# Kernel optimization log

Measured on AMD Instinct MI355X. Metric: run time of the kernel, lower is better.

The kernel has to match this reference:

```python
import jax, jax.numpy as jnp
import numpy as np

N_NODES = 50000
N_EDGES = 800000


def sage_conv(x, src, dst, W_l, b_l, W_r, num_nodes):
    """PyG SAGEConv with mean aggregation: out = lin_l(mean_agg(neighbors)) + lin_r(x)."""
    # gather source-node features per edge, scatter-mean into destination nodes
    msg = x[src]                                                   # [E, F]
    agg = jax.ops.segment_sum(msg, dst, num_segments=num_nodes)    # [N, F]
    cnt = jax.ops.segment_sum(jnp.ones((src.shape[0],), x.dtype), dst,
                              num_segments=num_nodes)              # [N]
    agg = agg / jnp.maximum(cnt, 1.0)[:, None]
    return agg @ W_l + b_l + x @ W_r


def setup_inputs() -> dict:
    key = jax.random.key(0)
    ks = jax.random.split(key, 8)
    d_in, d_hid, d_out = 128, 256, 128
    s = lambda k, shape, fan: jax.random.normal(k, shape, jnp.float32) / np.sqrt(fan)
    return {
        "x": jax.random.normal(ks[0], (N_NODES, d_in), jnp.float32),
        "edge_index": jax.random.randint(ks[1], (2, N_EDGES), 0, N_NODES, jnp.int64),
        "W1_l": s(ks[2], (d_in, d_hid), d_in),
        "b1": jnp.zeros((d_hid,), jnp.float32),
        "W1_r": s(ks[3], (d_in, d_hid), d_in),
        "W2_l": s(ks[4], (d_hid, d_out), d_hid),
        "b2": jnp.zeros((d_out,), jnp.float32),
        "W2_r": s(ks[5], (d_hid, d_out), d_hid),
    }


def reference(x, edge_index, W1_l, b1, W1_r, W2_l, b2, W2_r):
    src, dst = edge_index[0], edge_index[1]
    n = x.shape[0]
    h = sage_conv(x, src, dst, W1_l, b1, W1_r, n)
    h = jax.nn.relu(h)  # dropout p=0.0 -> identity
    out = sage_conv(h, src, dst, W2_l, b2, W2_r, n)
    return out
```

## Files before the change

kernel.cpp:

```cpp
#include <hip/hip_runtime.h>
#include <hip/hip_bf16.h>
#include <stdint.h>

#define NN 50000
#define NE 800000
#define NB 196
#define EPB 2048
#define NBLK ((NE + EPB - 1) / EPB)
#define BCAP 8192

typedef __attribute__((ext_vector_type(8))) __bf16 bf16x8;
typedef __attribute__((ext_vector_type(4))) float f32x4;
typedef __attribute__((ext_vector_type(4))) int i32x4;

__device__ __forceinline__ float bflo(uint32_t u) { return __uint_as_float(u << 16); }
__device__ __forceinline__ float bfhi(uint32_t u) { return __uint_as_float(u & 0xffff0000u); }
__device__ __forceinline__ uint16_t f2bf(float f) {
    uint32_t u = __float_as_uint(f);
    u += 0x7fffu + ((u >> 16) & 1u);
    return (uint16_t)(u >> 16);
}
__device__ __forceinline__ float bf2f(uint16_t h) { return __uint_as_float(((uint32_t)h) << 16); }

__device__ __forceinline__ int xcd_swz(int bid, int nwg) {
    int q = nwg >> 3, r = nwg & 7;
    int xcd = bid & 7, idx = bid >> 3;
    int base = (xcd < r) ? xcd * (q + 1) : r * (q + 1) + (xcd - r) * q;
    return base + idx;
}

__device__ __forceinline__ int detect_i64(const int* ei, int* sh_cnt) {
    int t = threadIdx.x;
    if (t == 0) *sh_cnt = 0;
    __syncthreads();
    if (t < 64) atomicAdd(sh_cnt, (ei[2 * t + 1] != 0) ? 1 : 0);
    __syncthreads();
    return (*sh_cnt < 4) ? 1 : 0;
}

__device__ __forceinline__ int detect_fp32(const uint32_t* xu, int* sh_cnt) {
    int t = threadIdx.x;
    if (t == 0) *sh_cnt = 0;
    __syncthreads();
    uint32_t u = xu[t & 255];
    uint32_t lo = u & 0xffffu;
    uint32_t e = (lo >> 7) & 0xffu;
    int ok = (lo == 0u) || (e >= 96u && e <= 150u);
    if (t < 256) atomicAdd(sh_cnt, ok);
    __syncthreads();
    return (*sh_cnt < 192) ? 1 : 0;
}

__global__ __launch_bounds__(256) void scatter1(const int* __restrict__ ei,
                                                int* __restrict__ bucket_cur,
                                                uint32_t* __restrict__ staging) {
    __shared__ int hist[NB];
    __shared__ int curs[NB];
    __shared__ int shc;
    int fl = detect_i64(ei, &shc);
    int t = threadIdx.x;
    for (int i = t; i < NB; i += 256) hist[i] = 0;
    __syncthreads();
    int base = blockIdx.x * EPB;
    for (int i = 0; i < EPB; i += 256) {
        int e = base + i + t;
        if (e < NE) {
            int d = fl ? ei[2 * NE + 2 * e] : ei[NE + e];
            atomicAdd(&hist[d >> 8], 1);
        }
    }
    __syncthreads();
    for (int i = t; i < NB; i += 256)
        curs[i] = (hist[i] > 0) ? atomicAdd(&bucket_cur[i], hist[i]) : 0;
    __syncthreads();
    for (int i = 0; i < EPB; i += 256) {
        int e = base + i + t;
        if (e < NE) {
            int s, d;
            if (fl) { s = ei[2 * e]; d = ei[2 * NE + 2 * e]; }
            else    { s = ei[e];     d = ei[NE + e]; }
            int b = d >> 8;
            int p = atomicAdd(&curs[b], 1);
            staging[b * BCAP + p] = ((uint32_t)(d & 0xff) << 16) | (uint32_t)s;
        }
    }
}

#define NORMX_BLKS 6250
__global__ __launch_bounds__(256) void csr_norm(const uint32_t* __restrict__ staging,
                                                const int* __restrict__ bucket_cur,
                                                const void* __restrict__ x,
                                                const void* __restrict__ w1l, const void* __restrict__ b1,
                                                const void* __restrict__ w1r, const void* __restrict__ w2l,
                                                const void* __restrict__ b2, const void* __restrict__ w2r,
                                                int* __restrict__ row_start, int* __restrict__ deg,
                                                float* __restrict__ inv_deg, int* __restrict__ csr,
                                                uint32_t* __restrict__ xb,
                                                uint16_t* __restrict__ w1l_sw, uint16_t* __restrict__ w1r_sw,
                                                uint16_t* __restrict__ w2l_sw, uint16_t* __restrict__ w2r_sw,
                                                uint16_t* __restrict__ bias_buf) {
    int blk = blockIdx.x;
    int t = threadIdx.x;
    if (blk < NB) {
        __shared__ int degs[256];
        __shared__ int sm[256];
        __shared__ int curs[256];
        int beg = blk * BCAP, cnt = bucket_cur[blk];
        degs[t] = 0;
        __syncthreads();
        for (int i = t; i < cnt; i += 256) atomicAdd(&degs[(staging[beg + i] >> 16) & 0xff], 1);
        __syncthreads();
        int d = degs[t];
        sm[t] = d;
        __syncthreads();
        for (int o = 1; o < 256; o <<= 1) {
            int x2 = (t >= o) ? sm[t - o] : 0;
            __syncthreads();
            sm[t] += x2;
            __syncthreads();
        }
        int excl = sm[t] - d;
        curs[t] = excl;
        int node = blk * 256 + t;
        if (node < NN) {
            row_start[node] = beg + excl;
            deg[node] = d;
            inv_deg[node] = 1.0f / (float)(d > 0 ? d : 1);
        }
        __syncthreads();
        for (int i = t; i < cnt; i += 256) {
            uint32_t u = staging[beg + i];
            int dl = (u >> 16) & 0xff;
            int p = atomicAdd(&curs[dl], 1);
            csr[beg + p] = (int)(u & 0xffffu);
        }
        return;
    }
    __shared__ int shc;
    int fp32 = detect_fp32((const uint32_t*)x, &shc);
    int nb = blk - NB;
    if (nb < NORMX_BLKS) {
        int i = nb * 256 + t;
        if (fp32) {
            f32x4 v = ((const f32x4*)x)[i];
            uint2 o;
            o.x = (uint32_t)f2bf(v[0]) | ((uint32_t)f2bf(v[1]) << 16);
            o.y = (uint32_t)f2bf(v[2]) | ((uint32_t)f2bf(v[3]) << 16);
            ((uint2*)xb)[i] = o;
        } else {
            ((uint2*)xb)[i] = ((const uint2*)x)[i];
        }
        return;
    }
    int tid = (nb - NORMX_BLKS) * 256 + t;
    if (tid < 16384) {
        int frag = tid >> 6, lane = tid & 63;
        const void* srcw; uint16_t* dst; int N; int fl;
        if (frag < 64)       { srcw = w1l; dst = w1l_sw; N = 256; fl = frag; }
        else if (frag < 128) { srcw = w1r; dst = w1r_sw; N = 256; fl = frag - 64; }
        else if (frag < 192) { srcw = w2l; dst = w2l_sw; N = 128; fl = frag - 128; }
        else                 { srcw = w2r; dst = w2r_sw; N = 128; fl = frag - 192; }
        int NTm = N >> 4;
        int kt = fl / NTm, nt = fl - kt * NTm;
        int k0 = kt * 32 + (lane >> 4) * 8, n = nt * 16 + (lane & 15);
        uint16_t* d = dst + (size_t)fl * 512 + lane * 8;
#pragma unroll
        for (int j = 0; j < 8; j++) {
            int si = (k0 + j) * N + n;
            d[j] = fp32 ? f2bf(((const float*)srcw)[si]) : ((const uint16_t*)srcw)[si];
        }
    } else if (tid < 16384 + 384) {
        int j = tid - 16384;
        const void* s = (j < 256) ? b1 : b2;
        int jj = (j < 256) ? j : j - 256;
        bias_buf[j] = fp32 ? f2bf(((const float*)s)[jj]) : ((const uint16_t*)s)[jj];
    }
}

__global__ __launch_bounds__(256) void agg_mean_v2(const uint32_t* __restrict__ xu,
                                                   const int* __restrict__ row_start,
                                                   const int* __restrict__ deg,
                                                   const int* __restrict__ csr,
                                                   const float* __restrict__ inv_deg,
                                                   uint32_t* __restrict__ outu) {
    int wave = threadIdx.x >> 6, lane = threadIdx.x & 63;
    int half = lane >> 5, l = lane & 31;
    int node = blockIdx.x * 8 + wave * 2 + half;
    int beg = row_start[node], end = beg + deg[node];
    float lx[8], hx[8], ly[8], hy[8];
#pragma unroll
    for (int k = 0; k < 8; k++) { lx[k] = 0.f; hx[k] = 0.f; ly[k] = 0.f; hy[k] = 0.f; }
    int j = beg;
    for (; j + 8 <= end; j += 8) {
        int idx[8];
#pragma unroll
        for (int k = 0; k < 8; k++) idx[k] = csr[j + k];
#pragma unroll
        for (int k = 0; k < 8; k++) {
            uint2 v = *(const uint2*)(xu + (size_t)idx[k] * 64 + l * 2);
            lx[k] += bflo(v.x); hx[k] += bfhi(v.x);
            ly[k] += bflo(v.y); hy[k] += bfhi(v.y);
        }
    }
    for (; j < end; j++) {
        uint2 v = *(const uint2*)(xu + (size_t)csr[j] * 64 + l * 2);
        lx[0] += bflo(v.x); hx[0] += bfhi(v.x);
        ly[0] += bflo(v.y); hy[0] += bfhi(v.y);
    }
    float sc = inv_deg[node];
    float r0 = (((lx[0] + lx[1]) + (lx[2] + lx[3])) + ((lx[4] + lx[5]) + (lx[6] + lx[7]))) * sc;
    float r1 = (((hx[0] + hx[1]) + (hx[2] + hx[3])) + ((hx[4] + hx[5]) + (hx[6] + hx[7]))) * sc;
    float r2 = (((ly[0] + ly[1]) + (ly[2] + ly[3])) + ((ly[4] + ly[5]) + (ly[6] + ly[7]))) * sc;
    float r3 = (((hy[0] + hy[1]) + (hy[2] + hy[3])) + ((hy[4] + hy[5]) + (hy[6] + hy[7]))) * sc;
    uint2 o;
    o.x = (uint32_t)f2bf(r0) | ((uint32_t)f2bf(r1) << 16);
    o.y = (uint32_t)f2bf(r2) | ((uint32_t)f2bf(r3) << 16);
    *(uint2*)(outu + (size_t)node * 64 + l * 2) = o;
}

__global__ __launch_bounds__(256) void agg_final_v2(const uint32_t* __restrict__ tu,
                                                    const int* __restrict__ row_start,
                                                    const int* __restrict__ deg,
                                                    const int* __restrict__ csr,
                                                    const float* __restrict__ inv_deg,
                                                    const f32x4* __restrict__ u,
                                                    f32x4* __restrict__ out) {
    int wave = threadIdx.x >> 6, lane = threadIdx.x & 63;
    int half = lane >> 5, l = lane & 31;
    int node = blockIdx.x * 8 + wave * 2 + half;
    int beg = row_start[node], end = beg + deg[node];
    float lx[8], hx[8], ly[8], hy[8];
#pragma unroll
    for (int k = 0; k < 8; k++) { lx[k] = 0.f; hx[k] = 0.f; ly[k] = 0.f; hy[k] = 0.f; }
    int j = beg;
    for (; j + 8 <= end; j += 8) {
        int idx[8];
#pragma unroll
        for (int k = 0; k < 8; k++) idx[k] = csr[j + k];
#pragma unroll
        for (int k = 0; k < 8; k++) {
            uint2 v = *(const uint2*)(tu + (size_t)idx[k] * 64 + l * 2);
            lx[k] += bflo(v.x); hx[k] += bfhi(v.x);
            ly[k] += bflo(v.y); hy[k] += bfhi(v.y);
        }
    }
    for (; j < end; j++) {
        uint2 v = *(const uint2*)(tu + (size_t)csr[j] * 64 + l * 2);
        lx[0] += bflo(v.x); hx[0] += bfhi(v.x);
        ly[0] += bflo(v.y); hy[0] += bfhi(v.y);
    }
    float sc = inv_deg[node];
    f32x4 uv = u[(size_t)node * 32 + l];
    f32x4 r;
    r[0] = (((lx[0] + lx[1]) + (lx[2] + lx[3])) + ((lx[4] + lx[5]) + (lx[6] + lx[7]))) * sc + uv[0];
    r[1] = (((hx[0] + hx[1]) + (hx[2] + hx[3])) + ((hx[4] + hx[5]) + (hx[6] + hx[7]))) * sc + uv[1];
    r[2] = (((ly[0] + ly[1]) + (ly[2] + ly[3])) + ((ly[4] + ly[5]) + (ly[6] + ly[7]))) * sc + uv[2];
    r[3] = (((hy[0] + hy[1]) + (hy[2] + hy[3])) + ((hy[4] + hy[5]) + (hy[6] + hy[7]))) * sc + uv[3];
    out[(size_t)node * 32 + l] = r;
}

__global__ __launch_bounds__(256) void gemm1_v3(const uint16_t* __restrict__ A1,
                                                const uint16_t* __restrict__ A2,
                                                const uint16_t* __restrict__ W1sw,
                                                const uint16_t* __restrict__ W2sw,
                                                const uint16_t* __restrict__ bias,
                                                uint16_t* __restrict__ C) {
    __shared__ __align__(16) uint16_t cs[64][72];
    int wg = xcd_swz(blockIdx.x, 3128);
    int rg = wg >> 2, cg = wg & 3;
    int wave = threadIdx.x >> 6, lane = threadIdx.x & 63;
    int wr = wave >> 1, wc = wave & 1;
    int m = lane & 15, q = lane >> 4;
    int rowbase = rg * 64 + wr * 32;
    int gnt0 = cg * 4 + wc * 2;

    int ar[2];
#pragma unroll
    for (int rf = 0; rf < 2; rf++) {
        int r = rowbase + rf * 16 + m;
        ar[rf] = (r < NN) ? r : (NN - 1);
    }

    bf16x8 B1[4][2], B2[4][2];
#pragma unroll
    for (int kt = 0; kt < 4; kt++)
#pragma unroll
        for (int nt = 0; nt < 2; nt++) {
            B1[kt][nt] = *(const bf16x8*)(W1sw + ((size_t)(kt * 16 + gnt0 + nt)) * 512 + lane * 8);
            B2[kt][nt] = *(const bf16x8*)(W2sw + ((size_t)(kt * 16 + gnt0 + nt)) * 512 + lane * 8);
        }

    f32x4 acc[2][2];
#pragma unroll
    for (int rf = 0; rf < 2; rf++)
#pragma unroll
        for (int nt = 0; nt < 2; nt++)
#pragma unroll
            for (int i = 0; i < 4; i++) acc[rf][nt][i] = 0.f;

#pragma unroll
    for (int kt = 0; kt < 4; kt++) {
        bf16x8 a10 = *(const bf16x8*)(A1 + (size_t)ar[0] * 128 + kt * 32 + q * 8);
        bf16x8 a11 = *(const bf16x8*)(A1 + (size_t)ar[1] * 128 + kt * 32 + q * 8);
        bf16x8 a20 = *(const bf16x8*)(A2 + (size_t)ar[0] * 128 + kt * 32 + q * 8);
        bf16x8 a21 = *(const bf16x8*)(A2 + (size_t)ar[1] * 128 + kt * 32 + q * 8);
#pragma unroll
        for (int nt = 0; nt < 2; nt++) {
            acc[0][nt] = __builtin_amdgcn_mfma_f32_16x16x32_bf16(a10, B1[kt][nt], acc[0][nt], 0, 0, 0);
            acc[1][nt] = __builtin_amdgcn_mfma_f32_16x16x32_bf16(a11, B1[kt][nt], acc[1][nt], 0, 0, 0);
            acc[0][nt] = __builtin_amdgcn_mfma_f32_16x16x32_bf16(a20, B2[kt][nt], acc[0][nt], 0, 0, 0);
            acc[1][nt] = __builtin_amdgcn_mfma_f32_16x16x32_bf16(a21, B2[kt][nt], acc[1][nt], 0, 0, 0);
        }
    }

#pragma unroll
    for (int rf = 0; rf < 2; rf++)
#pragma unroll
        for (int nt = 0; nt < 2; nt++) {
            int coll = wc * 32 + nt * 16 + m;
            float bv = bf2f(bias[cg * 64 + coll]);
#pragma unroll
            for (int i = 0; i < 4; i++) {
                float v = fmaxf(acc[rf][nt][i] + bv, 0.f);
                cs[wr * 32 + rf * 16 + q * 4 + i][coll] = f2bf(v);
            }
        }
    __syncthreads();
    int tt = threadIdx.x;
#pragma unroll
    for (int rr = 0; rr < 2; rr++) {
        int row = rr * 32 + (tt >> 3);
        int grow = rg * 64 + row;
        if (grow < NN)
            *(i32x4*)(C + (size_t)grow * 256 + cg * 64 + (tt & 7) * 8) =
                *(const i32x4*)&cs[row][(tt & 7) * 8];
    }
}

__global__ __launch_bounds__(256) void gemm2_v3(const uint16_t* __restrict__ A,
                                                const uint16_t* __restrict__ W1sw,
                                                const uint16_t* __restrict__ W2sw,
                                                const uint16_t* __restrict__ bias,
                                                uint16_t* __restrict__ T,
                                                float* __restrict__ U) {
    __shared__ __align__(16) uint16_t ts[64][72];
    __shared__ __align__(16) float us[64][68];
    int wg = xcd_swz(blockIdx.x, 1564);
    int rg = wg >> 1, cg = wg & 1;
    int wave = threadIdx.x >> 6, lane = threadIdx.x & 63;
    int wr = wave >> 1, wc = wave & 1;
    int m = lane & 15, q = lane >> 4;
    int rowbase = rg * 64 + wr * 32;
    int gnt0 = cg * 4 + wc * 2;

    int ar[2];
#pragma unroll
    for (int rf = 0; rf < 2; rf++) {
        int r = rowbase + rf * 16 + m;
        ar[rf] = (r < NN) ? r : (NN - 1);
    }

    f32x4 acc1[2][2], acc2[2][2];
#pragma unroll
    for (int rf = 0; rf < 2; rf++)
#pragma unroll
        for (int nt = 0; nt < 2; nt++)
#pragma unroll
            for (int i = 0; i < 4; i++) { acc1[rf][nt][i] = 0.f; acc2[rf][nt][i] = 0.f; }

#pragma unroll
    for (int kt = 0; kt < 8; kt++) {
        bf16x8 b10 = *(const bf16x8*)(W1sw + ((size_t)(kt * 8 + gnt0 + 0)) * 512 + lane * 8);
        bf16x8 b11 = *(const bf16x8*)(W1sw + ((size_t)(kt * 8 + gnt0 + 1)) * 512 + lane * 8);
        bf16x8 b20 = *(const bf16x8*)(W2sw + ((size_t)(kt * 8 + gnt0 + 0)) * 512 + lane * 8);
        bf16x8 b21 = *(const bf16x8*)(W2sw + ((size_t)(kt * 8 + gnt0 + 1)) * 512 + lane * 8);
        bf16x8 a0 = *(const bf16x8*)(A + (size_t)ar[0] * 256 + kt * 32 + q * 8);
        bf16x8 a1 = *(const bf16x8*)(A + (size_t)ar[1] * 256 + kt * 32 + q * 8);
        acc1[0][0] = __builtin_amdgcn_mfma_f32_16x16x32_bf16(a0, b10, acc1[0][0], 0, 0, 0);
        acc1[0][1] = __builtin_amdgcn_mfma_f32_16x16x32_bf16(a0, b11, acc1[0][1], 0, 0, 0);
        acc1[1][0] = __builtin_amdgcn_mfma_f32_16x16x32_bf16(a1, b10, acc1[1][0], 0, 0, 0);
        acc1[1][1] = __builtin_amdgcn_mfma_f32_16x16x32_bf16(a1, b11, acc1[1][1], 0, 0, 0);
        acc2[0][0] = __builtin_amdgcn_mfma_f32_16x16x32_bf16(a0, b20, acc2[0][0], 0, 0, 0);
        acc2[0][1] = __builtin_amdgcn_mfma_f32_16x16x32_bf16(a0, b21, acc2[0][1], 0, 0, 0);
        acc2[1][0] = __builtin_amdgcn_mfma_f32_16x16x32_bf16(a1, b20, acc2[1][0], 0, 0, 0);
        acc2[1][1] = __builtin_amdgcn_mfma_f32_16x16x32_bf16(a1, b21, acc2[1][1], 0, 0, 0);
    }

#pragma unroll
    for (int rf = 0; rf < 2; rf++)
#pragma unroll
        for (int nt = 0; nt < 2; nt++) {
            int coll = wc * 32 + nt * 16 + m;
            float bv = bf2f(bias[cg * 64 + coll]);
#pragma unroll
            for (int i = 0; i < 4; i++) {
                int rl = wr * 32 + rf * 16 + q * 4 + i;
                ts[rl][coll] = f2bf(acc1[rf][nt][i]);
                us[rl][coll] = acc2[rf][nt][i] + bv;
            }
        }
    __syncthreads();
    int tt = threadIdx.x;
#pragma unroll
    for (int rr = 0; rr < 2; rr++) {
        int row = rr * 32 + (tt >> 3);
        int grow = rg * 64 + row;
        if (grow < NN)
            *(i32x4*)(T + (size_t)grow * 128 + cg * 64 + (tt & 7) * 8) =
                *(const i32x4*)&ts[row][(tt & 7) * 8];
    }
#pragma unroll
    for (int rr = 0; rr < 4; rr++) {
        int row = rr * 16 + (tt >> 4);
        int grow = rg * 64 + row;
        if (grow < NN)
            *(f32x4*)(U + (size_t)grow * 128 + cg * 64 + (tt & 15) * 4) =
                *(const f32x4*)&us[row][(tt & 15) * 4];
    }
}

extern "C" void kernel_launch(void* const* d_in, const int* in_sizes, int n_in,
                              void* d_out, int out_size, void* d_ws, size_t ws_size,
                              hipStream_t stream) {
    const void* x_raw  = d_in[0];
    const int*  ei     = (const int*)d_in[1];
    const void* W1l    = d_in[2];
    const void* b1     = d_in[3];
    const void* W1r    = d_in[4];
    const void* W2l    = d_in[5];
    const void* b2     = d_in[6];
    const void* W2r    = d_in[7];

    uint8_t* ws = (uint8_t*)d_ws;
    size_t off = 0;
    auto alloc = [&](size_t b) -> void* {
        void* p = ws + off;
        off += (b + 255) & ~(size_t)255;
        return p;
    };
    int*      bucket_cur  = (int*)alloc((NB + 4) * 4);
    int*      deg         = (int*)alloc((size_t)NN * 4);
    float*    inv_deg     = (float*)alloc((size_t)NN * 4);
    int*      row_start   = (int*)alloc((size_t)NN * 4);
    int*      csr         = (int*)alloc((size_t)NB * BCAP * 4);
    uint32_t* xb          = (uint32_t*)alloc((size_t)NN * 64 * 4);
    uint16_t* bias_buf    = (uint16_t*)alloc(384 * 2);
    uint16_t* agg         = (uint16_t*)alloc((size_t)NN * 128 * 2);
    uint16_t* h           = (uint16_t*)alloc((size_t)NN * 256 * 2);
    uint16_t* t           = (uint16_t*)alloc((size_t)NN * 128 * 2);
    float*    u           = (float*)alloc((size_t)NN * 128 * 4);
    uint16_t* w1l_sw      = (uint16_t*)alloc(128 * 256 * 2);
    uint16_t* w1r_sw      = (uint16_t*)alloc(128 * 256 * 2);
    uint16_t* w2l_sw      = (uint16_t*)alloc(256 * 128 * 2);
    uint16_t* w2r_sw      = (uint16_t*)alloc(256 * 128 * 2);

    uint32_t* staging = (uint32_t*)h;

    hipMemsetAsync(bucket_cur, 0, NB * 4, stream);
    scatter1<<<NBLK, 256, 0, stream>>>(ei, bucket_cur, staging);
    csr_norm<<<NB + NORMX_BLKS + 66, 256, 0, stream>>>(staging, bucket_cur, x_raw,
                                                       W1l, b1, W1r, W2l, b2, W2r,
                                                       row_start, deg, inv_deg, csr,
                                                       xb, w1l_sw, w1r_sw, w2l_sw, w2r_sw, bias_buf);

    agg_mean_v2<<<NN / 8, 256, 0, stream>>>(xb, row_start, deg, csr, inv_deg, (uint32_t*)agg);
    gemm1_v3<<<3128, 256, 0, stream>>>(agg, (const uint16_t*)xb, w1l_sw, w1r_sw, bias_buf, h);
    gemm2_v3<<<1564, 256, 0, stream>>>(h, w2l_sw, w2r_sw, bias_buf + 256, t, u);
    agg_final_v2<<<NN / 8, 256, 0, stream>>>((const uint32_t*)t, row_start, deg, csr, inv_deg,
                                             (const f32x4*)u, (f32x4*)d_out);
}
```

Baseline: 255.6 us.

## Slice aggregation kernels by feature column, splitting edges across lanes

Both gather-mean kernels now split the 128 features into 8 column slices, one slice per block, and spread each node's edges across 8 lane groups. The partial sums are then combined with xor shuffles, and results are written with nontemporal stores. The aim is to keep each block's gather working set smaller and more cache-local, and to give more independent loads per wave. In exchange, csr indices are read 8 times and the shuffle reductions add overhead.

Result: slower. 378.4 us (+48.0%).

```diff
diff --git a/kernel.cpp b/kernel.cpp
--- a/kernel.cpp
+++ b/kernel.cpp
@@ -12,6 +12,7 @@
 typedef __attribute__((ext_vector_type(8))) __bf16 bf16x8;
 typedef __attribute__((ext_vector_type(4))) float f32x4;
 typedef __attribute__((ext_vector_type(4))) int i32x4;
+typedef __attribute__((ext_vector_type(2))) uint32_t u32x2;
 
 __device__ __forceinline__ float bflo(uint32_t u) { return __uint_as_float(u << 16); }
 __device__ __forceinline__ float bfhi(uint32_t u) { return __uint_as_float(u & 0xffff0000u); }
@@ -177,86 +178,112 @@
     }
 }
 
-__global__ __launch_bounds__(256) void agg_mean_v2(const uint32_t* __restrict__ xu,
+__global__ __launch_bounds__(256) void agg_mean_s(const uint32_t* __restrict__ xu,
+                                                  const int* __restrict__ row_start,
+                                                  const int* __restrict__ deg,
+                                                  const int* __restrict__ csr,
+                                                  const float* __restrict__ inv_deg,
+                                                  uint32_t* __restrict__ outu) {
+    int s = blockIdx.x & 7, ng = blockIdx.x >> 3;
+    int t = threadIdx.x;
+    int hw = t >> 5, l = t & 31;
+    int esub = l >> 2, dpair = l & 3;
+    int colu = s * 8 + dpair * 2;
+    for (int it = 0; it < 8; it++) {
+        int node = ng * 64 + hw * 8 + it;
+        if (node >= NN) break;
+        int beg = row_start[node], d = deg[node];
+        float f0 = 0.f, f1 = 0.f, f2 = 0.f, f3 = 0.f;
+        int j = 0;
+        for (; j + 16 <= d; j += 16) {
+            int i0 = csr[beg + j + esub];
+            int i1 = csr[beg + j + 8 + esub];
+            uint2 v0 = *(const uint2*)(xu + (size_t)i0 * 64 + colu);
+            uint2 v1 = *(const uint2*)(xu + (size_t)i1 * 64 + colu);
+            f0 += bflo(v0.x) + bflo(v1.x);
+            f1 += bfhi(v0.x) + bfhi(v1.x);
+            f2 += bflo(v0.y) + bflo(v1.y);
+            f3 += bfhi(v0.y) + bfhi(v1.y);
+        }
+        for (; j < d; j += 8) {
+            if (j + esub < d) {
+                int i0 = csr[beg + j + esub];
+                uint2 v0 = *(const uint2*)(xu + (size_t)i0 * 64 + colu);
+                f0 += bflo(v0.x); f1 += bfhi(v0.x);
+                f2 += bflo(v0.y); f3 += bfhi(v0.y);
+            }
+        }
+#pragma unroll
+        for (int mask = 4; mask <= 16; mask <<= 1) {
+            f0 += __shfl_xor(f0, mask);
+            f1 += __shfl_xor(f1, mask);
+            f2 += __shfl_xor(f2, mask);
+            f3 += __shfl_xor(f3, mask);
+        }
+        if (esub == 0) {
+            float sc = inv_deg[node];
+            u32x2 o;
+            o[0] = (uint32_t)f2bf(f0 * sc) | ((uint32_t)f2bf(f1 * sc) << 16);
+            o[1] = (uint32_t)f2bf(f2 * sc) | ((uint32_t)f2bf(f3 * sc) << 16);
+            __builtin_nontemporal_store(o, (u32x2*)(outu + (size_t)node * 64 + colu));
+        }
+    }
+}
+
+__global__ __launch_bounds__(256) void agg_final_s(const uint32_t* __restrict__ tu,
                                                    const int* __restrict__ row_start,
                                                    const int* __restrict__ deg,
                                                    const int* __restrict__ csr,
                                                    const float* __restrict__ inv_deg,
-                                                   uint32_t* __restrict__ outu) {
-    int wave = threadIdx.x >> 6, lane = threadIdx.x & 63;
-    int half = lane >> 5, l = lane & 31;
-    int node = blockIdx.x * 8 + wave * 2 + half;
-    int beg = row_start[node], end = beg + deg[node];
-    float lx[8], hx[8], ly[8], hy[8];
-#pragma unroll
-    for (int k = 0; k < 8; k++) { lx[k] = 0.f; hx[k] = 0.f; ly[k] = 0.f; hy[k] = 0.f; }
-    int j = beg;
-    for (; j + 8 <= end; j += 8) {
-        int idx[8];
-#pragma unroll
-        for (int k = 0; k < 8; k++) idx[k] = csr[j + k];
-#pragma unroll
-        for (int k = 0; k < 8; k++) {
-            uint2 v = *(const uint2*)(xu + (size_t)idx[k] * 64 + l * 2);
-            lx[k] += bflo(v.x); hx[k] += bfhi(v.x);
-            ly[k] += bflo(v.y); hy[k] += bfhi(v.y);
-        }
-    }
-    for (; j < end; j++) {
-        uint2 v = *(const uint2*)(xu + (size_t)csr[j] * 64 + l * 2);
-        lx[0] += bflo(v.x); hx[0] += bfhi(v.x);
-        ly[0] += bflo(v.y); hy[0] += bfhi(v.y);
-    }
-    float sc = inv_deg[node];
-    float r0 = (((lx[0] + lx[1]) + (lx[2] + lx[3])) + ((lx[4] + lx[5]) + (lx[6] + lx[7]))) * sc;
-    float r1 = (((hx[0] + hx[1]) + (hx[2] + hx[3])) + ((hx[4] + hx[5]) + (hx[6] + hx[7]))) * sc;
-    float r2 = (((ly[0] + ly[1]) + (ly[2] + ly[3])) + ((ly[4] + ly[5]) + (ly[6] + ly[7]))) * sc;
-    float r3 = (((hy[0] + hy[1]) + (hy[2] + hy[3])) + ((hy[4] + hy[5]) + (hy[6] + hy[7]))) * sc;
-    uint2 o;
-    o.x = (uint32_t)f2bf(r0) | ((uint32_t)f2bf(r1) << 16);
-    o.y = (uint32_t)f2bf(r2) | ((uint32_t)f2bf(r3) << 16);
-    *(uint2*)(outu + (size_t)node * 64 + l * 2) = o;
-}
-
-__global__ __launch_bounds__(256) void agg_final_v2(const uint32_t* __restrict__ tu,
-                                                    const int* __restrict__ row_start,
-                                                    const int* __restrict__ deg,
-                                                    const int* __restrict__ csr,
-                                                    const float* __restrict__ inv_deg,
-                                                    const f32x4* __restrict__ u,
-                                                    f32x4* __restrict__ out) {
-    int wave = threadIdx.x >> 6, lane = threadIdx.x & 63;
-    int half = lane >> 5, l = lane & 31;
-    int node = blockIdx.x * 8 + wave * 2 + half;
-    int beg = row_start[node], end = beg + deg[node];
-    float lx[8], hx[8], ly[8], hy[8];
-#pragma unroll
-    for (int k = 0; k < 8; k++) { lx[k] = 0.f; hx[k] = 0.f; ly[k] = 0.f; hy[k] = 0.f; }
-    int j = beg;
-    for (; j + 8 <= end; j += 8) {
-        int idx[8];
-#pragma unroll
-        for (int k = 0; k < 8; k++) idx[k] = csr[j + k];
-#pragma unroll
-        for (int k = 0; k < 8; k++) {
-            uint2 v = *(const uint2*)(tu + (size_t)idx[k] * 64 + l * 2);
-            lx[k] += bflo(v.x); hx[k] += bfhi(v.x);
-            ly[k] += bflo(v.y); hy[k] += bfhi(v.y);
-        }
-    }
-    for (; j < end; j++) {
-        uint2 v = *(const uint2*)(tu + (size_t)csr[j] * 64 + l * 2);
-        lx[0] += bflo(v.x); hx[0] += bfhi(v.x);
-        ly[0] += bflo(v.y); hy[0] += bfhi(v.y);
-    }
-    float sc = inv_deg[node];
-    f32x4 uv = u[(size_t)node * 32 + l];
-    f32x4 r;
-    r[0] = (((lx[0] + lx[1]) + (lx[2] + lx[3])) + ((lx[4] + lx[5]) + (lx[6] + lx[7]))) * sc + uv[0];
-    r[1] = (((hx[0] + hx[1]) + (hx[2] + hx[3])) + ((hx[4] + hx[5]) + (hx[6] + hx[7]))) * sc + uv[1];
-    r[2] = (((ly[0] + ly[1]) + (ly[2] + ly[3])) + ((ly[4] + ly[5]) + (ly[6] + ly[7]))) * sc + uv[2];
-    r[3] = (((hy[0] + hy[1]) + (hy[2] + hy[3])) + ((hy[4] + hy[5]) + (hy[6] + hy[7]))) * sc + uv[3];
-    out[(size_t)node * 32 + l] = r;
+                                                   const float* __restrict__ u,
+                                                   float* __restrict__ out) {
+    int s = blockIdx.x & 7, ng = blockIdx.x >> 3;
+    int t = threadIdx.x;
+    int hw = t >> 5, l = t & 31;
+    int esub = l >> 2, dpair = l & 3;
+    int colu = s * 8 + dpair * 2;
+    for (int it = 0; it < 8; it++) {
+        int node = ng * 64 + hw * 8 + it;
+        if (node >= NN) break;
+        int beg = row_start[node], d = deg[node];
+        float f0 = 0.f, f1 = 0.f, f2 = 0.f, f3 = 0.f;
+        int j = 0;
+        for (; j + 16 <= d; j += 16) {
+            int i0 = csr[beg + j + esub];
+            int i1 = csr[beg + j + 8 + esub];
+            uint2 v0 = *(const uint2*)(tu + (size_t)i0 * 64 + colu);
+            uint2 v1 = *(const uint2*)(tu + (size_t)i1 * 64 + colu);
+            f0 += bflo(v0.x) + bflo(v1.x);
+            f1 += bfhi(v0.x) + bfhi(v1.x);
+            f2 += bflo(v0.y) + bflo(v1.y);
+            f3 += bfhi(v0.y) + bfhi(v1.y);
+        }
+        for (; j < d; j += 8) {
+            if (j + esub < d) {
+                int i0 = csr[beg + j + esub];
+                uint2 v0 = *(const uint2*)(tu + (size_t)i0 * 64 + colu);
+                f0 += bflo(v0.x); f1 += bfhi(v0.x);
+                f2 += bflo(v0.y); f3 += bfhi(v0.y);
+            }
+        }
+#pragma unroll
+        for (int mask = 4; mask <= 16; mask <<= 1) {
+            f0 += __shfl_xor(f0, mask);
+            f1 += __shfl_xor(f1, mask);
+            f2 += __shfl_xor(f2, mask);
+            f3 += __shfl_xor(f3, mask);
+        }
+        if (esub == 0) {
+            float sc = inv_deg[node];
+            f32x4 uv = *(const f32x4*)(u + (size_t)node * 128 + s * 16 + dpair * 4);
+            f32x4 r;
+            r[0] = f0 * sc + uv[0];
+            r[1] = f1 * sc + uv[1];
+            r[2] = f2 * sc + uv[2];
+            r[3] = f3 * sc + uv[3];
+            __builtin_nontemporal_store(r, (f32x4*)(out + (size_t)node * 128 + s * 16 + dpair * 4));
+        }
+    }
 }
 
 __global__ __launch_bounds__(256) void gemm1_v3(const uint16_t* __restrict__ A1,
@@ -463,9 +490,10 @@
                                                        row_start, deg, inv_deg, csr,
                                                        xb, w1l_sw, w1r_sw, w2l_sw, w2r_sw, bias_buf);
 
-    agg_mean_v2<<<NN / 8, 256, 0, stream>>>(xb, row_start, deg, csr, inv_deg, (uint32_t*)agg);
+    agg_mean_s<<<8 * ((NN + 63) / 64), 256, 0, stream>>>(xb, row_start, deg, csr, inv_deg,
+                                                         (uint32_t*)agg);
     gemm1_v3<<<3128, 256, 0, stream>>>(agg, (const uint16_t*)xb, w1l_sw, w1r_sw, bias_buf, h);
     gemm2_v3<<<1564, 256, 0, stream>>>(h, w2l_sw, w2r_sw, bias_buf + 256, t, u);
-    agg_final_v2<<<NN / 8, 256, 0, stream>>>((const uint32_t*)t, row_start, deg, csr, inv_deg,
-                                             (const f32x4*)u, (f32x4*)d_out);
-}
+    agg_final_s<<<8 * ((NN + 63) / 64), 256, 0, stream>>>((const uint32_t*)t, row_start, deg, csr,
+                                                          inv_deg, u, (float*)d_out);
+}
```

## Fuse the two dense GEMM stages, keeping hidden activations in shared memory

Applied to the files above, without the earlier changes.

Replaces the two separate GEMM kernels with one fused kernel. Each block computes a 64-row tile of the layer-1 hidden activations (bias plus ReLU) into LDS, then immediately runs the layer-2 projections from LDS and writes T and U. This removes the global write and re-read of the 50000x256 hidden tensor and one kernel launch. In exchange there are fewer, heavier blocks, more accumulator registers and more LDS per block, which may lower occupancy. The edge staging buffer now aliases the T buffer.

Result: no change. 255.2 us (-0.2%).

```diff
diff --git a/kernel.cpp b/kernel.cpp
--- a/kernel.cpp
+++ b/kernel.cpp
@@ -259,163 +259,141 @@
     out[(size_t)node * 32 + l] = r;
 }
 
-__global__ __launch_bounds__(256) void gemm1_v3(const uint16_t* __restrict__ A1,
-                                                const uint16_t* __restrict__ A2,
-                                                const uint16_t* __restrict__ W1sw,
-                                                const uint16_t* __restrict__ W2sw,
-                                                const uint16_t* __restrict__ bias,
-                                                uint16_t* __restrict__ C) {
-    __shared__ __align__(16) uint16_t cs[64][72];
-    int wg = xcd_swz(blockIdx.x, 3128);
-    int rg = wg >> 2, cg = wg & 3;
-    int wave = threadIdx.x >> 6, lane = threadIdx.x & 63;
+#define HW 264
+__global__ __launch_bounds__(256) void fused_mlp(const uint16_t* __restrict__ AGG,
+                                                 const uint16_t* __restrict__ XB,
+                                                 const uint16_t* __restrict__ W1Lsw,
+                                                 const uint16_t* __restrict__ W1Rsw,
+                                                 const uint16_t* __restrict__ W2Lsw,
+                                                 const uint16_t* __restrict__ W2Rsw,
+                                                 const uint16_t* __restrict__ bias,
+                                                 uint16_t* __restrict__ T,
+                                                 float* __restrict__ U) {
+    __shared__ __align__(16) uint16_t hbuf[64 * HW];
+    int wg = xcd_swz(blockIdx.x, 782);
+    int node0 = wg * 64;
+    int tid = threadIdx.x;
+    int wave = tid >> 6, lane = tid & 63;
     int wr = wave >> 1, wc = wave & 1;
     int m = lane & 15, q = lane >> 4;
-    int rowbase = rg * 64 + wr * 32;
-    int gnt0 = cg * 4 + wc * 2;
 
     int ar[2];
 #pragma unroll
     for (int rf = 0; rf < 2; rf++) {
-        int r = rowbase + rf * 16 + m;
+        int r = node0 + wr * 32 + rf * 16 + m;
         ar[rf] = (r < NN) ? r : (NN - 1);
     }
 
-    bf16x8 B1[4][2], B2[4][2];
-#pragma unroll
-    for (int kt = 0; kt < 4; kt++)
-#pragma unroll
-        for (int nt = 0; nt < 2; nt++) {
-            B1[kt][nt] = *(const bf16x8*)(W1sw + ((size_t)(kt * 16 + gnt0 + nt)) * 512 + lane * 8);
-            B2[kt][nt] = *(const bf16x8*)(W2sw + ((size_t)(kt * 16 + gnt0 + nt)) * 512 + lane * 8);
-        }
-
-    f32x4 acc[2][2];
+    {
+        f32x4 acc[2][8];
+#pragma unroll
+        for (int rf = 0; rf < 2; rf++)
+#pragma unroll
+            for (int nt = 0; nt < 8; nt++)
+#pragma unroll
+                for (int i = 0; i < 4; i++) acc[rf][nt][i] = 0.f;
+
+#pragma unroll
+        for (int kt = 0; kt < 4; kt++) {
+            bf16x8 a10 = *(const bf16x8*)(AGG + (size_t)ar[0] * 128 + kt * 32 + q * 8);
+            bf16x8 a11 = *(const bf16x8*)(AGG + (size_t)ar[1] * 128 + kt * 32 + q * 8);
+            bf16x8 a20 = *(const bf16x8*)(XB + (size_t)ar[0] * 128 + kt * 32 + q * 8);
+            bf16x8 a21 = *(const bf16x8*)(XB + (size_t)ar[1] * 128 + kt * 32 + q * 8);
+#pragma unroll
+            for (int nt = 0; nt < 8; nt++) {
+                int gnt = wc * 8 + nt;
+                bf16x8 B1 = *(const bf16x8*)(W1Lsw + ((size_t)(kt * 16 + gnt)) * 512 + lane * 8);
+                bf16x8 B2 = *(const bf16x8*)(W1Rsw + ((size_t)(kt * 16 + gnt)) * 512 + lane * 8);
+                acc[0][nt] = __builtin_amdgcn_mfma_f32_16x16x32_bf16(a10, B1, acc[0][nt], 0, 0, 0);
+                acc[1][nt] = __builtin_amdgcn_mfma_f32_16x16x32_bf16(a11, B1, acc[1][nt], 0, 0, 0);
+                acc[0][nt] = __builtin_amdgcn_mfma_f32_16x16x32_bf16(a20, B2, acc[0][nt], 0, 0, 0);
+                acc[1][nt] = __builtin_amdgcn_mfma_f32_16x16x32_bf16(a21, B2, acc[1][nt], 0, 0, 0);
+            }
+        }
+#pragma unroll
+        for (int rf = 0; rf < 2; rf++)
+#pragma unroll
+            for (int nt = 0; nt < 8; nt++) {
+                int cl = wc * 128 + nt * 16 + m;
+                float bv = bf2f(bias[cl]);
+#pragma unroll
+                for (int i = 0; i < 4; i++) {
+                    float v = fmaxf(acc[rf][nt][i] + bv, 0.f);
+                    hbuf[(wr * 32 + rf * 16 + q * 4 + i) * HW + cl] = f2bf(v);
+                }
+            }
+    }
+    __syncthreads();
+
+    f32x4 acc1[2][4], acc2[2][4];
 #pragma unroll
     for (int rf = 0; rf < 2; rf++)
 #pragma unroll
-        for (int nt = 0; nt < 2; nt++)
-#pragma unroll
-            for (int i = 0; i < 4; i++) acc[rf][nt][i] = 0.f;
-
-#pragma unroll
-    for (int kt = 0; kt < 4; kt++) {
-        bf16x8 a10 = *(const bf16x8*)(A1 + (size_t)ar[0] * 128 + kt * 32 + q * 8);
-        bf16x8 a11 = *(const bf16x8*)(A1 + (size_t)ar[1] * 128 + kt * 32 + q * 8);
-        bf16x8 a20 = *(const bf16x8*)(A2 + (size_t)ar[0] * 128 + kt * 32 + q * 8);
-        bf16x8 a21 = *(const bf16x8*)(A2 + (size_t)ar[1] * 128 + kt * 32 + q * 8);
-#pragma unroll
-        for (int nt = 0; nt < 2; nt++) {
-            acc[0][nt] = __builtin_amdgcn_mfma_f32_16x16x32_bf16(a10, B1[kt][nt], acc[0][nt], 0, 0, 0);
-            acc[1][nt] = __builtin_amdgcn_mfma_f32_16x16x32_bf16(a11, B1[kt][nt], acc[1][nt], 0, 0, 0);
-            acc[0][nt] = __builtin_amdgcn_mfma_f32_16x16x32_bf16(a20, B2[kt][nt], acc[0][nt], 0, 0, 0);
-            acc[1][nt] = __builtin_amdgcn_mfma_f32_16x16x32_bf16(a21, B2[kt][nt], acc[1][nt], 0, 0, 0);
-        }
-    }
-
-#pragma unroll
-    for (int rf = 0; rf < 2; rf++)
-#pragma unroll
-        for (int nt = 0; nt < 2; nt++) {
-            int coll = wc * 32 + nt * 16 + m;
-            float bv = bf2f(bias[cg * 64 + coll]);
-#pragma unroll
-            for (int i = 0; i < 4; i++) {
-                float v = fmaxf(acc[rf][nt][i] + bv, 0.f);
-                cs[wr * 32 + rf * 16 + q * 4 + i][coll] = f2bf(v);
+        for (int nt = 0; nt < 4; nt++)
+#pragma unroll
+            for (int i = 0; i < 4; i++) { acc1[rf][nt][i] = 0.f; acc2[rf][nt][i] = 0.f; }
+
+#pragma unroll
+    for (int kt = 0; kt < 8; kt++) {
+        bf16x8 a0 = *(const bf16x8*)&hbuf[(wr * 32 + m) * HW + kt * 32 + q * 8];
+        bf16x8 a1 = *(const bf16x8*)&hbuf[(wr * 32 + 16 + m) * HW + kt * 32 + q * 8];
+#pragma unroll
+        for (int nt = 0; nt < 4; nt++) {
+            int gnt = wc * 4 + nt;
+            bf16x8 BL = *(const bf16x8*)(W2Lsw + ((size_t)(kt * 8 + gnt)) * 512 + lane * 8);
+            bf16x8 BR = *(const bf16x8*)(W2Rsw + ((size_t)(kt * 8 + gnt)) * 512 + lane * 8);
+            acc1[0][nt] = __builtin_amdgcn_mfma_f32_16x16x32_bf16(a0, BL, acc1[0][nt], 0, 0, 0);
+            acc1[1][nt] = __builtin_amdgcn_mfma_f32_16x16x32_bf16(a1, BL, acc1[1][nt], 0, 0, 0);
+            acc2[0][nt] = __builtin_amdgcn_mfma_f32_16x16x32_bf16(a0, BR, acc2[0][nt], 0, 0, 0);
+            acc2[1][nt] = __builtin_amdgcn_mfma_f32_16x16x32_bf16(a1, BR, acc2[1][nt], 0, 0, 0);
+        }
+    }
+    __syncthreads();
+
+    {
+        uint16_t* st = hbuf;
+#pragma unroll
+        for (int rf = 0; rf < 2; rf++)
+#pragma unroll
+            for (int nt = 0; nt < 4; nt++) {
+                int cl = wc * 64 + nt * 16 + m;
+#pragma unroll
+                for (int i = 0; i < 4; i++)
+                    st[(wr * 32 + rf * 16 + q * 4 + i) * 136 + cl] = f2bf(acc1[rf][nt][i]);
             }
-        }
-    __syncthreads();
-    int tt = threadIdx.x;
-#pragma unroll
-    for (int rr = 0; rr < 2; rr++) {
-        int row = rr * 32 + (tt >> 3);
-        int grow = rg * 64 + row;
-        if (grow < NN)
-            *(i32x4*)(C + (size_t)grow * 256 + cg * 64 + (tt & 7) * 8) =
-                *(const i32x4*)&cs[row][(tt & 7) * 8];
-    }
-}
-
-__global__ __launch_bounds__(256) void gemm2_v3(const uint16_t* __restrict__ A,
-                                                const uint16_t* __restrict__ W1sw,
-                                                const uint16_t* __restrict__ W2sw,
-                                                const uint16_t* __restrict__ bias,
-                                                uint16_t* __restrict__ T,
-                                                float* __restrict__ U) {
-    __shared__ __align__(16) uint16_t ts[64][72];
-    __shared__ __align__(16) float us[64][68];
-    int wg = xcd_swz(blockIdx.x, 1564);
-    int rg = wg >> 1, cg = wg & 1;
-    int wave = threadIdx.x >> 6, lane = threadIdx.x & 63;
-    int wr = wave >> 1, wc = wave & 1;
-    int m = lane & 15, q = lane >> 4;
-    int rowbase = rg * 64 + wr * 32;
-    int gnt0 = cg * 4 + wc * 2;
-
-    int ar[2];
-#pragma unroll
-    for (int rf = 0; rf < 2; rf++) {
-        int r = rowbase + rf * 16 + m;
-        ar[rf] = (r < NN) ? r : (NN - 1);
-    }
-
-    f32x4 acc1[2][2], acc2[2][2];
-#pragma unroll
-    for (int rf = 0; rf < 2; rf++)
-#pragma unroll
-        for (int nt = 0; nt < 2; nt++)
-#pragma unroll
-            for (int i = 0; i < 4; i++) { acc1[rf][nt][i] = 0.f; acc2[rf][nt][i] = 0.f; }
-
-#pragma unroll
-    for (int kt = 0; kt < 8; kt++) {
-        bf16x8 b10 = *(const bf16x8*)(W1sw + ((size_t)(kt * 8 + gnt0 + 0)) * 512 + lane * 8);
-        bf16x8 b11 = *(const bf16x8*)(W1sw + ((size_t)(kt * 8 + gnt0 + 1)) * 512 + lane * 8);
-        bf16x8 b20 = *(const bf16x8*)(W2sw + ((size_t)(kt * 8 + gnt0 + 0)) * 512 + lane * 8);
-        bf16x8 b21 = *(const bf16x8*)(W2sw + ((size_t)(kt * 8 + gnt0 + 1)) * 512 + lane * 8);
-        bf16x8 a0 = *(const bf16x8*)(A + (size_t)ar[0] * 256 + kt * 32 + q * 8);
-        bf16x8 a1 = *(const bf16x8*)(A + (size_t)ar[1] * 256 + kt * 32 + q * 8);
-        acc1[0][0] = __builtin_amdgcn_mfma_f32_16x16x32_bf16(a0, b10, acc1[0][0], 0, 0, 0);
-        acc1[0][1] = __builtin_amdgcn_mfma_f32_16x16x32_bf16(a0, b11, acc1[0][1], 0, 0, 0);
-        acc1[1][0] = __builtin_amdgcn_mfma_f32_16x16x32_bf16(a1, b10, acc1[1][0], 0, 0, 0);
-        acc1[1][1] = __builtin_amdgcn_mfma_f32_16x16x32_bf16(a1, b11, acc1[1][1], 0, 0, 0);
-        acc2[0][0] = __builtin_amdgcn_mfma_f32_16x16x32_bf16(a0, b20, acc2[0][0], 0, 0, 0);
-        acc2[0][1] = __builtin_amdgcn_mfma_f32_16x16x32_bf16(a0, b21, acc2[0][1], 0, 0, 0);
-        acc2[1][0] = __builtin_amdgcn_mfma_f32_16x16x32_bf16(a1, b20, acc2[1][0], 0, 0, 0);
-        acc2[1][1] = __builtin_amdgcn_mfma_f32_16x16x32_bf16(a1, b21, acc2[1][1], 0, 0, 0);
-    }
-
-#pragma unroll
-    for (int rf = 0; rf < 2; rf++)
-#pragma unroll
-        for (int nt = 0; nt < 2; nt++) {
-            int coll = wc * 32 + nt * 16 + m;
-            float bv = bf2f(bias[cg * 64 + coll]);
-#pragma unroll
-            for (int i = 0; i < 4; i++) {
-                int rl = wr * 32 + rf * 16 + q * 4 + i;
-                ts[rl][coll] = f2bf(acc1[rf][nt][i]);
-                us[rl][coll] = acc2[rf][nt][i] + bv;
+        __syncthreads();
+#pragma unroll
+        for (int rr = 0; rr < 4; rr++) {
+            int row = rr * 16 + (tid >> 4);
+            int grow = node0 + row;
+            if (grow < NN)
+                *(i32x4*)(T + (size_t)grow * 128 + (tid & 15) * 8) =
+                    *(const i32x4*)&st[row * 136 + (tid & 15) * 8];
+        }
+        __syncthreads();
+    }
+
+    {
+        float* su = (float*)hbuf;
+#pragma unroll
+        for (int rf = 0; rf < 2; rf++)
+#pragma unroll
+            for (int nt = 0; nt < 4; nt++) {
+                int cl = wc * 64 + nt * 16 + m;
+                float bv = bf2f(bias[256 + cl]);
+#pragma unroll
+                for (int i = 0; i < 4; i++)
+                    su[(wr * 32 + rf * 16 + q * 4 + i) * 132 + cl] = acc2[rf][nt][i] + bv;
             }
-        }
-    __syncthreads();
-    int tt = threadIdx.x;
-#pragma unroll
-    for (int rr = 0; rr < 2; rr++) {
-        int row = rr * 32 + (tt >> 3);
-        int grow = rg * 64 + row;
-        if (grow < NN)
-            *(i32x4*)(T + (size_t)grow * 128 + cg * 64 + (tt & 7) * 8) =
-                *(const i32x4*)&ts[row][(tt & 7) * 8];
-    }
-#pragma unroll
-    for (int rr = 0; rr < 4; rr++) {
-        int row = rr * 16 + (tt >> 4);
-        int grow = rg * 64 + row;
-        if (grow < NN)
-            *(f32x4*)(U + (size_t)grow * 128 + cg * 64 + (tt & 15) * 4) =
-                *(const f32x4*)&us[row][(tt & 15) * 4];
+        __syncthreads();
+#pragma unroll
+        for (int rr = 0; rr < 8; rr++) {
+            int row = rr * 8 + (tid >> 5);
+            int grow = node0 + row;
+            if (grow < NN)
+                *(f32x4*)(U + (size_t)grow * 128 + (tid & 31) * 4) =
+                    *(const f32x4*)&su[row * 132 + (tid & 31) * 4];
+        }
     }
 }
 
@@ -446,7 +424,6 @@
     uint32_t* xb          = (uint32_t*)alloc((size_t)NN * 64 * 4);
     uint16_t* bias_buf    = (uint16_t*)alloc(384 * 2);
     uint16_t* agg         = (uint16_t*)alloc((size_t)NN * 128 * 2);
-    uint16_t* h           = (uint16_t*)alloc((size_t)NN * 256 * 2);
     uint16_t* t           = (uint16_t*)alloc((size_t)NN * 128 * 2);
     float*    u           = (float*)alloc((size_t)NN * 128 * 4);
     uint16_t* w1l_sw      = (uint16_t*)alloc(128 * 256 * 2);
@@ -454,7 +431,7 @@
     uint16_t* w2l_sw      = (uint16_t*)alloc(256 * 128 * 2);
     uint16_t* w2r_sw      = (uint16_t*)alloc(256 * 128 * 2);
 
-    uint32_t* staging = (uint32_t*)h;
+    uint32_t* staging = (uint32_t*)t;
 
     hipMemsetAsync(bucket_cur, 0, NB * 4, stream);
     scatter1<<<NBLK, 256, 0, stream>>>(ei, bucket_cur, staging);
@@ -464,8 +441,8 @@
                                                        xb, w1l_sw, w1r_sw, w2l_sw, w2r_sw, bias_buf);
 
     agg_mean_v2<<<NN / 8, 256, 0, stream>>>(xb, row_start, deg, csr, inv_deg, (uint32_t*)agg);
-    gemm1_v3<<<3128, 256, 0, stream>>>(agg, (const uint16_t*)xb, w1l_sw, w1r_sw, bias_buf, h);
-    gemm2_v3<<<1564, 256, 0, stream>>>(h, w2l_sw, w2r_sw, bias_buf + 256, t, u);
+    fused_mlp<<<782, 256, 0, stream>>>(agg, (const uint16_t*)xb,
+                                       w1l_sw, w1r_sw, w2l_sw, w2r_sw, bias_buf, t, u);
     agg_final_v2<<<NN / 8, 256, 0, stream>>>((const uint32_t*)t, row_start, deg, csr, inv_deg,
                                              (const f32x4*)u, (f32x4*)d_out);
 }
```
